# Performance work log

Measured on AMD Instinct MI355X. Metric: run time of the kernel, lower is better.

## Reference

```python
import jax, jax.numpy as jnp
import numpy as np

B = 16384
WIDE_DIM = 256          # 32 wide features * dim 8
DEEP_DIM = 1024         # 64 deep features * embedding_dim 16
SHARED = [2048, 1024, 512]
DOMAIN = [512, 256]
NUM_DOMAINS = 8


def setup_inputs() -> dict:
    key = jax.random.key(0)
    ks = jax.random.split(key, 20)
    s = 0.01  # embedding_init_var-style small init
    inp = {
        "wide_features": jax.random.normal(ks[0], (B, WIDE_DIM), jnp.float32),
        "deep_features": jax.random.normal(ks[1], (B, DEEP_DIM), jnp.float32),
        "domain_ids": jax.random.randint(ks[2], (B,), 0, NUM_DOMAINS, jnp.int64),
        # shared MLP (weights stored [in, out])
        "W1": jax.random.normal(ks[3], (DEEP_DIM, SHARED[0]), jnp.float32) * s,
        "b1": jnp.zeros((SHARED[0],), jnp.float32),
        "W2": jax.random.normal(ks[4], (SHARED[0], SHARED[1]), jnp.float32) * s,
        "b2": jnp.zeros((SHARED[1],), jnp.float32),
        "W3": jax.random.normal(ks[5], (SHARED[1], SHARED[2]), jnp.float32) * s,
        "b3": jnp.zeros((SHARED[2],), jnp.float32),
        # domain-specific MLP
        "Wd1": jax.random.normal(ks[6], (SHARED[2], DOMAIN[0]), jnp.float32) * s,
        "bd1": jnp.zeros((DOMAIN[0],), jnp.float32),
        "Wd2": jax.random.normal(ks[7], (DOMAIN[0], DOMAIN[1]), jnp.float32) * s,
        "bd2": jnp.zeros((DOMAIN[1],), jnp.float32),
        # per-domain output heads: Linear(DOMAIN[-1], 1) per domain
        "Wh": jax.random.normal(ks[8], (NUM_DOMAINS, DOMAIN[1]), jnp.float32) * s,
        "bh": jnp.zeros((NUM_DOMAINS,), jnp.float32),
    }
    return inp


def reference(wide_features, deep_features, domain_ids,
              W1, b1, W2, b2, W3, b3, Wd1, bd1, Wd2, bd2, Wh, bh):
    # wide part: sum embedding output to a scalar logit per sample [B, 1]
    wide = jnp.sum(wide_features, axis=1, keepdims=True)
    # shared deep MLP
    h = jax.nn.relu(deep_features @ W1 + b1)
    h = jax.nn.relu(h @ W2 + b2)
    shared = jax.nn.relu(h @ W3 + b3)          # [B, 512]
    # domain-specific tower (shared across domains)
    d = jax.nn.relu(shared @ Wd1 + bd1)
    d = jax.nn.relu(d @ Wd2 + bd2)             # [B, 256]
    # per-sample domain head routing: gather head weights, fused dot
    w = Wh[domain_ids]                          # [B, 256]
    head = jnp.sum(d * w, axis=1, keepdims=True) + bh[domain_ids][:, None]  # [B, 1]
    out = jax.nn.sigmoid(wide + head)
    return (out, shared, d)
```

## Files before the change

kernel.cpp:

```cpp
#include <hip/hip_runtime.h>
#include <hip/hip_bf16.h>


typedef __attribute__((ext_vector_type(8))) short short8;
typedef __attribute__((ext_vector_type(4))) float f32x4;

static __device__ __forceinline__ unsigned short f2bf_bits(float x) {
  __hip_bfloat16 h = __float2bfloat16(x);
  return __builtin_bit_cast(unsigned short, h);
}
static __device__ __forceinline__ float bf_bits2f(unsigned short u) {
  __hip_bfloat16 h = __builtin_bit_cast(__hip_bfloat16, u);
  return __bfloat162float(h);
}

static __device__ __forceinline__ void gload16(const void* g, void* l) {
  __builtin_amdgcn_global_load_lds(
      (const __attribute__((address_space(1))) void*)g,
      (__attribute__((address_space(3))) void*)l, 16, 0, 0);
}

static __device__ __forceinline__ unsigned lds_u32(const void* p) {
  return (unsigned)(uintptr_t)(const __attribute__((address_space(3))) void*)p;
}

static __device__ __forceinline__ short8 dsr(unsigned addr) {
  short8 r;
  asm volatile("ds_read_b128 %0, %1" : "=v"(r) : "v"(addr));
  return r;
}

#define MFMA16(a, b, c) __builtin_amdgcn_mfma_f32_16x16x32_bf16((a), (b), (c), 0, 0, 0)
#define SB0() __builtin_amdgcn_sched_barrier(0)
#define PRIO(x) __builtin_amdgcn_s_setprio(x)
#define BAR() __builtin_amdgcn_s_barrier()

__global__ void transpose_convert(const float* __restrict__ W,
                                  __hip_bfloat16* __restrict__ Wt,
                                  int K, int N) {
  __shared__ float tile[64][65];
  const int k0 = blockIdx.y * 64;
  const int n0 = blockIdx.x * 64;
  const int t  = threadIdx.x;
  const int tn = t & 63;
  const int t4 = t >> 6;
#pragma unroll
  for (int p = 0; p < 16; ++p) {
    int kl = p * 4 + t4;
    tile[kl][tn] = W[(size_t)(k0 + kl) * N + (n0 + tn)];
  }
  __syncthreads();
#pragma unroll
  for (int p = 0; p < 16; ++p) {
    int nl = p * 4 + t4;
    Wt[(size_t)(n0 + nl) * K + (k0 + tn)] = __float2bfloat16(tile[tn][nl]);
  }
}

__global__ void f32_to_bf16(const float* __restrict__ in,
                            unsigned short* __restrict__ out, int n8) {
  int i = blockIdx.x * blockDim.x + threadIdx.x;
  if (i >= n8) return;
  const f32x4* p = (const f32x4*)in + (size_t)i * 2;
  f32x4 a = p[0], b = p[1];
  short8 o;
  o[0] = (short)f2bf_bits(a[0]); o[1] = (short)f2bf_bits(a[1]);
  o[2] = (short)f2bf_bits(a[2]); o[3] = (short)f2bf_bits(a[3]);
  o[4] = (short)f2bf_bits(b[0]); o[5] = (short)f2bf_bits(b[1]);
  o[6] = (short)f2bf_bits(b[2]); o[7] = (short)f2bf_bits(b[3]);
  *(short8*)(out + (size_t)i * 8) = o;
}

__global__ __launch_bounds__(512, 2) void gemm_8p(
    const __hip_bfloat16* __restrict__ A,
    const __hip_bfloat16* __restrict__ Bt,
    const float* __restrict__ bias,
    __hip_bfloat16* __restrict__ Cb,
    float* __restrict__ Cf,
    int N, int K, int nbx) {
  __shared__ char lds[131072];

  const int tid  = threadIdx.x;
  const int lane = tid & 63;
  const int wid  = tid >> 6;
  const int wm   = wid >> 2;
  const int wn   = wid & 3;

  const int nwg = gridDim.x;
  const int cpx = nwg >> 3;
  const int id  = blockIdx.x;
  const int swz = (id & 7) * cpx + (id >> 3);
  const int bm  = (swz / nbx) * 256;
  const int bn  = (swz % nbx) * 256;

  const int ln15 = lane & 15;
  const unsigned cswz = (unsigned)((((lane >> 4) ^ (lane & 7)) << 4));

  const unsigned lbase = lds_u32(lds);
  const unsigned arow0 = lbase + (unsigned)(wm * 128 + ln15) * 128u + cswz;
  const unsigned brow0 = lbase + 32768u + (unsigned)(wn * 64 + ln15) * 128u + cswz;

  const int nt = K >> 6;

  const int swc = (tid & 7) ^ ((tid >> 3) & 7);
  const __hip_bfloat16* baseA = A  + (size_t)(bm + (tid >> 3)) * K + swc * 8;
  const __hip_bfloat16* baseB = Bt + (size_t)(bn + (tid >> 3)) * K + swc * 8;
  const unsigned ldst0 = (unsigned)(wid * 1024);

  auto stage = [&](int kt, int half, int isB) {
    const __hip_bfloat16* base = isB ? baseB : baseA;
    char* dst = lds + ((kt & 1) * 65536) + (isB ? 32768 : 0) + half * 16384;
#pragma unroll
    for (int q = 0; q < 2; ++q) {
      gload16(base + (size_t)((half * 128 + q * 64) * K + kt * 64),
              dst + q * 8192 + ldst0);
    }
  };

  f32x4 acc[8][4] = {};

  stage(0, 0, 1); stage(0, 0, 0); stage(0, 1, 1); stage(0, 1, 0);
  if (nt > 1) { stage(1, 0, 1); stage(1, 0, 0); }

  for (int t = 0; t < nt; ++t) {
    const unsigned po = (unsigned)(t & 1) * 65536u;
    short8 a_[4][2], b0_[2][2], b1_[2][2];

    if (t + 1 < nt) asm volatile("s_waitcnt vmcnt(4)");
    else            asm volatile("s_waitcnt vmcnt(0)");
    BAR();
#pragma unroll
    for (int mi = 0; mi < 4; ++mi) a_[mi][0] = dsr(arow0 + po + (unsigned)(mi * 2048));
#pragma unroll
    for (int nj = 0; nj < 2; ++nj) b0_[nj][0] = dsr(brow0 + po + (unsigned)(nj * 2048));
#pragma unroll
    for (int mi = 0; mi < 4; ++mi) a_[mi][1] = dsr((arow0 + po + (unsigned)(mi * 2048)) ^ 64u);
#pragma unroll
    for (int nj = 0; nj < 2; ++nj) b0_[nj][1] = dsr((brow0 + po + (unsigned)(nj * 2048)) ^ 64u);
    if (t + 1 < nt) stage(t + 1, 1, 1);
    asm volatile("s_waitcnt lgkmcnt(6)");
    SB0();
    PRIO(1);
#pragma unroll
    for (int mi = 0; mi < 4; ++mi)
#pragma unroll
      for (int nj = 0; nj < 2; ++nj)
        acc[mi][nj] = MFMA16(a_[mi][0], b0_[nj][0], acc[mi][nj]);
    asm volatile("s_waitcnt lgkmcnt(0)");
    SB0();
#pragma unroll
    for (int mi = 0; mi < 4; ++mi)
#pragma unroll
      for (int nj = 0; nj < 2; ++nj)
        acc[mi][nj] = MFMA16(a_[mi][1], b0_[nj][1], acc[mi][nj]);
    PRIO(0);

#pragma unroll
    for (int nj = 0; nj < 2; ++nj) {
      unsigned bd = brow0 + po + (unsigned)((nj + 2) * 2048);
      b1_[nj][0] = dsr(bd); b1_[nj][1] = dsr(bd ^ 64u);
    }
    if (t + 1 < nt) stage(t + 1, 1, 0);
    BAR();
    asm volatile("s_waitcnt lgkmcnt(0)");
    SB0();
    PRIO(1);
#pragma unroll
    for (int kk = 0; kk < 2; ++kk)
#pragma unroll
      for (int mi = 0; mi < 4; ++mi)
#pragma unroll
        for (int nj = 0; nj < 2; ++nj)
          acc[mi][nj + 2] = MFMA16(a_[mi][kk], b1_[nj][kk], acc[mi][nj + 2]);
    PRIO(0);

#pragma unroll
    for (int mi = 0; mi < 4; ++mi) {
      unsigned ad = arow0 + po + (unsigned)((mi + 4) * 2048);
      a_[mi][0] = dsr(ad); a_[mi][1] = dsr(ad ^ 64u);
    }
    BAR();
    if (t + 2 < nt) stage(t + 2, 0, 1);
    asm volatile("s_waitcnt lgkmcnt(0)");
    SB0();
    PRIO(1);
#pragma unroll
    for (int kk = 0; kk < 2; ++kk)
#pragma unroll
      for (int mi = 0; mi < 4; ++mi)
#pragma unroll
        for (int nj = 0; nj < 2; ++nj)
          acc[mi + 4][nj] = MFMA16(a_[mi][kk], b0_[nj][kk], acc[mi + 4][nj]);
    PRIO(0);

    BAR();
    if (t + 2 < nt) stage(t + 2, 0, 0);
    PRIO(1);
#pragma unroll
    for (int kk = 0; kk < 2; ++kk)
#pragma unroll
      for (int mi = 0; mi < 4; ++mi)
#pragma unroll
        for (int nj = 0; nj < 2; ++nj)
          acc[mi + 4][nj + 2] = MFMA16(a_[mi][kk], b1_[nj][kk], acc[mi + 4][nj + 2]);
    PRIO(0);
  }

  float biasv[4];
#pragma unroll
  for (int nj = 0; nj < 4; ++nj)
    biasv[nj] = bias[bn + wn * 64 + nj * 16 + ln15];

#pragma unroll
  for (int mi = 0; mi < 8; ++mi) {
    int row0 = bm + wm * 128 + mi * 16 + (lane >> 4) * 4;
#pragma unroll
    for (int nj = 0; nj < 4; ++nj) {
      int col = bn + wn * 64 + nj * 16 + ln15;
#pragma unroll
      for (int r = 0; r < 4; ++r) {
        float v = acc[mi][nj][r] + biasv[nj];
        v = v > 0.f ? v : 0.f;
        size_t idx = (size_t)(row0 + r) * N + col;
        Cb[idx] = __float2bfloat16(v);
        if (Cf) Cf[idx] = v;
      }
    }
  }
}

__global__ __launch_bounds__(512, 2) void gemm_8pq(
    const __hip_bfloat16* __restrict__ A,
    const __hip_bfloat16* __restrict__ Bt,
    const float* __restrict__ bias,
    __hip_bfloat16* __restrict__ Cb,
    int N, int K, int nbx) {
  __shared__ char lds[131072];

  const int tid  = threadIdx.x;
  const int lane = tid & 63;
  const int wid  = tid >> 6;
  const int wm   = wid >> 2;
  const int wn   = wid & 3;

  const int nwg = gridDim.x;
  const int cpx = nwg >> 3;
  const int id  = blockIdx.x;
  const int swz = (id & 7) * cpx + (id >> 3);
  const int bm  = (swz / nbx) * 256;
  const int bn  = (swz % nbx) * 256;

  const int ln15 = lane & 15;
  const unsigned cswz = (unsigned)((((lane >> 4) ^ (lane & 7)) << 4));

  const unsigned lbase = lds_u32(lds);
  const unsigned arow0 = lbase + (unsigned)(wm * 128 + ln15) * 128u + cswz;
  const unsigned brow0 = lbase + 32768u + (unsigned)(wn * 64 + ln15) * 128u + cswz;

  const int nt = K >> 6;

  const int swc = (tid & 7) ^ ((tid >> 3) & 7);
  const __hip_bfloat16* baseA = A  + (size_t)(bm + (tid >> 3)) * K + swc * 8;
  const __hip_bfloat16* baseB = Bt + (size_t)(bn + (tid >> 3)) * K + swc * 8;
  const unsigned ldst0 = (unsigned)(wid * 1024);

  auto stage = [&](int kt, int half, int isB) {
    const __hip_bfloat16* base = isB ? baseB : baseA;
    char* dst = lds + ((kt & 1) * 65536) + (isB ? 32768 : 0) + half * 16384;
#pragma unroll
    for (int q = 0; q < 2; ++q) {
      gload16(base + (size_t)((half * 128 + q * 64) * K + kt * 64),
              dst + q * 8192 + ldst0);
    }
  };

  f32x4 acc[8][4] = {};
  short8 aLo[4][2], aHi[4][2], b0v[2][2], b1v[2][2];

  stage(0, 0, 1); stage(0, 0, 0); stage(0, 1, 1); stage(0, 1, 0);
  if (nt > 1) {
    stage(1, 0, 1); stage(1, 0, 0);
    asm volatile("s_waitcnt vmcnt(4)");
  } else {
    asm volatile("s_waitcnt vmcnt(0)");
  }
  BAR();
#pragma unroll
  for (int mi = 0; mi < 4; ++mi) {
    unsigned ad = arow0 + (unsigned)(mi * 2048);
    aLo[mi][0] = dsr(ad); aLo[mi][1] = dsr(ad ^ 64u);
  }

  for (int t = 0; t < nt; ++t) {
    const unsigned po = (unsigned)(t & 1) * 65536u;
    const unsigned pn = po ^ 65536u;

    asm volatile("s_waitcnt lgkmcnt(0)");
    SB0();
#pragma unroll
    for (int nj = 0; nj < 2; ++nj) b0v[nj][0] = dsr(brow0 + po + (unsigned)(nj * 2048));
#pragma unroll
    for (int nj = 0; nj < 2; ++nj) b0v[nj][1] = dsr((brow0 + po + (unsigned)(nj * 2048)) ^ 64u);
#pragma unroll
    for (int nj = 0; nj < 2; ++nj) b1v[nj][0] = dsr(brow0 + po + (unsigned)((nj + 2) * 2048));
#pragma unroll
    for (int nj = 0; nj < 2; ++nj) b1v[nj][1] = dsr((brow0 + po + (unsigned)((nj + 2) * 2048)) ^ 64u);
    asm volatile("s_waitcnt lgkmcnt(6)");
    SB0();
    PRIO(1);
#pragma unroll
    for (int mi = 0; mi < 4; ++mi)
#pragma unroll
      for (int nj = 0; nj < 2; ++nj)
        acc[mi][nj] = MFMA16(aLo[mi][0], b0v[nj][0], acc[mi][nj]);
    asm volatile("s_waitcnt lgkmcnt(4)");
    SB0();
#pragma unroll
    for (int mi = 0; mi < 4; ++mi)
#pragma unroll
      for (int nj = 0; nj < 2; ++nj)
        acc[mi][nj] = MFMA16(aLo[mi][1], b0v[nj][1], acc[mi][nj]);
    PRIO(0);
    if (t + 1 < nt) stage(t + 1, 1, 1);
    BAR();

    asm volatile("s_waitcnt lgkmcnt(0)");
    SB0();
#pragma unroll
    for (int mi = 0; mi < 4; ++mi) {
      unsigned ad = arow0 + po + (unsigned)((mi + 4) * 2048);
      aHi[mi][0] = dsr(ad); aHi[mi][1] = dsr(ad ^ 64u);
    }
    PRIO(1);
#pragma unroll
    for (int kk = 0; kk < 2; ++kk)
#pragma unroll
      for (int mi = 0; mi < 4; ++mi)
#pragma unroll
        for (int nj = 0; nj < 2; ++nj)
          acc[mi][nj + 2] = MFMA16(aLo[mi][kk], b1v[nj][kk], acc[mi][nj + 2]);
    PRIO(0);
    if (t + 1 < nt) stage(t + 1, 1, 0);
    BAR();

    asm volatile("s_waitcnt lgkmcnt(0)");
    SB0();
    PRIO(1);
#pragma unroll
    for (int kk = 0; kk < 2; ++kk)
#pragma unroll
      for (int mi = 0; mi < 4; ++mi)
#pragma unroll
        for (int nj = 0; nj < 2; ++nj)
          acc[mi + 4][nj] = MFMA16(aHi[mi][kk], b0v[nj][kk], acc[mi + 4][nj]);
    PRIO(0);
    if (t + 2 < nt) stage(t + 2, 0, 1);
    if (t + 1 < nt) {
      if (t + 2 < nt) asm volatile("s_waitcnt vmcnt(2)");
      else            asm volatile("s_waitcnt vmcnt(0)");
    }
    BAR();

    SB0();
    if (t + 1 < nt) {
#pragma unroll
      for (int mi = 0; mi < 4; ++mi) {
        unsigned ad = arow0 + pn + (unsigned)(mi * 2048);
        aLo[mi][0] = dsr(ad); aLo[mi][1] = dsr(ad ^ 64u);
      }
    }
    PRIO(1);
#pragma unroll
    for (int kk = 0; kk < 2; ++kk)
#pragma unroll
      for (int mi = 0; mi < 4; ++mi)
#pragma unroll
        for (int nj = 0; nj < 2; ++nj)
          acc[mi + 4][nj + 2] = MFMA16(aHi[mi][kk], b1v[nj][kk], acc[mi + 4][nj + 2]);
    PRIO(0);
    if (t + 2 < nt) stage(t + 2, 0, 0);
    BAR();
  }

  float biasv[4];
#pragma unroll
  for (int nj = 0; nj < 4; ++nj)
    biasv[nj] = bias[bn + wn * 64 + nj * 16 + ln15];

#pragma unroll
  for (int mi = 0; mi < 8; ++mi) {
    int row0 = bm + wm * 128 + mi * 16 + (lane >> 4) * 4;
#pragma unroll
    for (int nj = 0; nj < 4; ++nj) {
      int col = bn + wn * 64 + nj * 16 + ln15;
#pragma unroll
      for (int r = 0; r < 4; ++r) {
        float v = acc[mi][nj][r] + biasv[nj];
        v = v > 0.f ? v : 0.f;
        Cb[(size_t)(row0 + r) * N + col] = __float2bfloat16(v);
      }
    }
  }
}

__global__ __launch_bounds__(512, 2) void gemm_128(
    const __hip_bfloat16* __restrict__ A,
    const __hip_bfloat16* __restrict__ Bt,
    const float* __restrict__ bias,
    __hip_bfloat16* __restrict__ Cb,
    float* __restrict__ Cf,
    int N, int K, int nbx) {
  __shared__ char lds[98304];

  const int tid  = threadIdx.x;
  const int lane = tid & 63;
  const int wid  = tid >> 6;
  const int wm   = wid >> 2;
  const int wn   = wid & 3;

  const int nwg = gridDim.x;
  const int cpx = nwg >> 3;
  const int id  = blockIdx.x;
  const int swz = (id & 7) * cpx + (id >> 3);
  const int bm  = (swz / nbx) * 128;
  const int bn  = (swz % nbx) * 256;

  const int ln15 = lane & 15;
  const unsigned cswz = (unsigned)((((lane >> 4) ^ (lane & 7)) << 4));

  const unsigned lbase = lds_u32(lds);
  const unsigned arow0 = lbase + (unsigned)(wm * 64 + ln15) * 128u + cswz;
  const unsigned brow0 = lbase + 16384u + (unsigned)(wn * 64 + ln15) * 128u + cswz;

  const int nt = K >> 6;

  const int swc = (tid & 7) ^ ((tid >> 3) & 7);
  const __hip_bfloat16* baseA = A  + (size_t)(bm + (tid >> 3)) * K + swc * 8;
  const __hip_bfloat16* baseB = Bt + (size_t)(bn + (tid >> 3)) * K + swc * 8;
  const unsigned ldst0 = (unsigned)(tid * 16);

  auto stageA = [&](int kt, int half) {
    char* dst = lds + ((kt & 1) * 49152) + half * 8192;
    gload16(baseA + (size_t)((half * 64) * K + kt * 64), dst + ldst0);
  };
  auto stageB = [&](int kt, int half) {
    char* dst = lds + ((kt & 1) * 49152) + 16384 + half * 16384;
#pragma unroll
    for (int q = 0; q < 2; ++q) {
      gload16(baseB + (size_t)((half * 128 + q * 64) * K + kt * 64),
              dst + q * 8192 + ldst0);
    }
  };

  f32x4 acc[4][4] = {};

  stageB(0, 0); stageA(0, 0); stageB(0, 1); stageA(0, 1);
  if (nt > 1) { stageB(1, 0); stageA(1, 0); }

  for (int t = 0; t < nt; ++t) {
    const unsigned po = (unsigned)(t & 1) * 49152u;
    short8 a_[4][2], b_[4][2];

    if (t + 1 < nt) asm volatile("s_waitcnt vmcnt(3)");
    else            asm volatile("s_waitcnt vmcnt(0)");
    BAR();
#pragma unroll
    for (int mi = 0; mi < 2; ++mi) a_[mi][0] = dsr(arow0 + po + (unsigned)(mi * 2048));
#pragma unroll
    for (int nj = 0; nj < 2; ++nj) b_[nj][0] = dsr(brow0 + po + (unsigned)(nj * 2048));
#pragma unroll
    for (int mi = 0; mi < 2; ++mi) a_[mi][1] = dsr((arow0 + po + (unsigned)(mi * 2048)) ^ 64u);
#pragma unroll
    for (int nj = 0; nj < 2; ++nj) b_[nj][1] = dsr((brow0 + po + (unsigned)(nj * 2048)) ^ 64u);
    if (t + 1 < nt) stageB(t + 1, 1);
    asm volatile("s_waitcnt lgkmcnt(4)");
    SB0();
    PRIO(1);
#pragma unroll
    for (int mi = 0; mi < 2; ++mi)
#pragma unroll
      for (int nj = 0; nj < 2; ++nj)
        acc[mi][nj] = MFMA16(a_[mi][0], b_[nj][0], acc[mi][nj]);
    asm volatile("s_waitcnt lgkmcnt(0)");
    SB0();
#pragma unroll
    for (int mi = 0; mi < 2; ++mi)
#pragma unroll
      for (int nj = 0; nj < 2; ++nj)
        acc[mi][nj] = MFMA16(a_[mi][1], b_[nj][1], acc[mi][nj]);
    PRIO(0);

#pragma unroll
    for (int nj = 0; nj < 2; ++nj) {
      unsigned bd = brow0 + po + (unsigned)((nj + 2) * 2048);
      b_[nj + 2][0] = dsr(bd); b_[nj + 2][1] = dsr(bd ^ 64u);
    }
    if (t + 1 < nt) stageA(t + 1, 1);
    BAR();
    asm volatile("s_waitcnt lgkmcnt(0)");
    SB0();
    PRIO(1);
#pragma unroll
    for (int kk = 0; kk < 2; ++kk)
#pragma unroll
      for (int mi = 0; mi < 2; ++mi)
#pragma unroll
        for (int nj = 0; nj < 2; ++nj)
          acc[mi][nj + 2] = MFMA16(a_[mi][kk], b_[nj + 2][kk], acc[mi][nj + 2]);
    PRIO(0);

#pragma unroll
    for (int mi = 0; mi < 2; ++mi) {
      unsigned ad = arow0 + po + (unsigned)((mi + 2) * 2048);
      a_[mi + 2][0] = dsr(ad); a_[mi + 2][1] = dsr(ad ^ 64u);
    }
    BAR();
    if (t + 2 < nt) stageB(t + 2, 0);
    asm volatile("s_waitcnt lgkmcnt(0)");
    SB0();
    PRIO(1);
#pragma unroll
    for (int kk = 0; kk < 2; ++kk)
#pragma unroll
      for (int mi = 0; mi < 2; ++mi)
#pragma unroll
        for (int nj = 0; nj < 2; ++nj)
          acc[mi + 2][nj] = MFMA16(a_[mi + 2][kk], b_[nj][kk], acc[mi + 2][nj]);
    PRIO(0);

    BAR();
    if (t + 2 < nt) stageA(t + 2, 0);
    PRIO(1);
#pragma unroll
    for (int kk = 0; kk < 2; ++kk)
#pragma unroll
      for (int mi = 0; mi < 2; ++mi)
#pragma unroll
        for (int nj = 0; nj < 2; ++nj)
          acc[mi + 2][nj + 2] = MFMA16(a_[mi + 2][kk], b_[nj + 2][kk], acc[mi + 2][nj + 2]);
    PRIO(0);
  }

  float biasv[4];
#pragma unroll
  for (int nj = 0; nj < 4; ++nj)
    biasv[nj] = bias[bn + wn * 64 + nj * 16 + ln15];

#pragma unroll
  for (int mi = 0; mi < 4; ++mi) {
    int row0 = bm + wm * 64 + mi * 16 + (lane >> 4) * 4;
#pragma unroll
    for (int nj = 0; nj < 4; ++nj) {
      int col = bn + wn * 64 + nj * 16 + ln15;
#pragma unroll
      for (int r = 0; r < 4; ++r) {
        float v = acc[mi][nj][r] + biasv[nj];
        v = v > 0.f ? v : 0.f;
        size_t idx = (size_t)(row0 + r) * N + col;
        Cb[idx] = __float2bfloat16(v);
        if (Cf) Cf[idx] = v;
      }
    }
  }
}

__global__ __launch_bounds__(256, 2) void gemm_bt(
    const __hip_bfloat16* __restrict__ A,
    const __hip_bfloat16* __restrict__ Bt,
    const float* __restrict__ bias,
    __hip_bfloat16* __restrict__ Cb,
    float* __restrict__ Cf,
    int N, int K) {
  __shared__ char lds[32768];

  const int tid  = threadIdx.x;
  const int lane = tid & 63;
  const int wid  = tid >> 6;
  const int wm   = wid >> 1;
  const int wn   = wid & 1;
  const int bm   = blockIdx.y * 128;
  const int bn   = blockIdx.x * 128;

  f32x4 acc[4][4] = {};

  const int srow = tid >> 3;
  const int sk   = (tid & 7) * 8;
  const int kTiles = K >> 6;

  for (int kt = 0; kt < kTiles; ++kt) {
    __syncthreads();
    const __hip_bfloat16* ga = A  + (size_t)(bm + srow) * K + kt * 64 + sk;
    const __hip_bfloat16* gb = Bt + (size_t)(bn + srow) * K + kt * 64 + sk;
#pragma unroll
    for (int p = 0; p < 4; ++p) {
      gload16(ga + (size_t)(p * 32) * K, &lds[p * 4096 + wid * 1024]);
      gload16(gb + (size_t)(p * 32) * K, &lds[16384 + p * 4096 + wid * 1024]);
    }
    __syncthreads();

#pragma unroll
    for (int kk = 0; kk < 2; ++kk) {
      short8 avec[4], bvec[4];
#pragma unroll
      for (int i = 0; i < 4; ++i) {
        int row = wm * 64 + i * 16 + (lane & 15);
        avec[i] = *(const short8*)&lds[row * 128 + kk * 64 + (lane >> 4) * 16];
      }
#pragma unroll
      for (int j = 0; j < 4; ++j) {
        int row = wn * 64 + j * 16 + (lane & 15);
        bvec[j] = *(const short8*)&lds[16384 + row * 128 + kk * 64 + (lane >> 4) * 16];
      }
#pragma unroll
      for (int i = 0; i < 4; ++i)
#pragma unroll
        for (int j = 0; j < 4; ++j)
          acc[i][j] = MFMA16(avec[i], bvec[j], acc[i][j]);
    }
  }

  float biasv[4];
#pragma unroll
  for (int j = 0; j < 4; ++j)
    biasv[j] = bias[bn + wn * 64 + j * 16 + (lane & 15)];

#pragma unroll
  for (int i = 0; i < 4; ++i) {
    int row0 = bm + wm * 64 + i * 16 + (lane >> 4) * 4;
#pragma unroll
    for (int j = 0; j < 4; ++j) {
      int col = bn + wn * 64 + j * 16 + (lane & 15);
#pragma unroll
      for (int r = 0; r < 4; ++r) {
        float v = acc[i][j][r] + biasv[j];
        v = v > 0.f ? v : 0.f;
        size_t idx = (size_t)(row0 + r) * N + col;
        Cb[idx] = __float2bfloat16(v);
        if (Cf) Cf[idx] = v;
      }
    }
  }
}

__global__ __launch_bounds__(256) void head_kernel(
    const float* __restrict__ wide,
    const __hip_bfloat16* __restrict__ D,
    const int* __restrict__ dom,
    const float* __restrict__ Wh,
    const float* __restrict__ bh,
    float* __restrict__ out, int B) {
  const int wid  = threadIdx.x >> 6;
  const int lane = threadIdx.x & 63;
  const int row  = blockIdx.x * 4 + wid;
  if (row >= B) return;
  const int dm = dom[row];

  f32x4 wv = ((const f32x4*)(wide + (size_t)row * 256))[lane];
  float tot = wv[0] + wv[1] + wv[2] + wv[3];

  const unsigned short* drow = (const unsigned short*)(D + (size_t)row * 256);
  ushort4 dv = ((const ushort4*)drow)[lane];
  f32x4 hv = ((const f32x4*)(Wh + (size_t)dm * 256))[lane];
  tot += bf_bits2f(dv.x) * hv[0] + bf_bits2f(dv.y) * hv[1] +
         bf_bits2f(dv.z) * hv[2] + bf_bits2f(dv.w) * hv[3];

#pragma unroll
  for (int off = 32; off > 0; off >>= 1) tot += __shfl_xor(tot, off);

  if (lane == 0) {
    float x = tot + bh[dm];
    out[row] = 1.f / (1.f + __expf(-x));
  }
}

extern "C" void kernel_launch(void* const* d_in, const int* in_sizes, int n_in,
                              void* d_out, int out_size, void* d_ws, size_t ws_size,
                              hipStream_t stream) {
  const float* wide = (const float*)d_in[0];
  const float* deep = (const float*)d_in[1];
  const int*   dom  = (const int*)d_in[2];
  const float* W1  = (const float*)d_in[3];
  const float* b1  = (const float*)d_in[4];
  const float* W2  = (const float*)d_in[5];
  const float* b2  = (const float*)d_in[6];
  const float* W3  = (const float*)d_in[7];
  const float* b3  = (const float*)d_in[8];
  const float* Wd1 = (const float*)d_in[9];
  const float* bd1 = (const float*)d_in[10];
  const float* Wd2 = (const float*)d_in[11];
  const float* bd2 = (const float*)d_in[12];
  const float* Wh  = (const float*)d_in[13];
  const float* bh  = (const float*)d_in[14];
  float* out = (float*)d_out;

  const int B = 16384;
  char* ws = (char*)d_ws;
  __hip_bfloat16* buf0 = (__hip_bfloat16*)ws;
  __hip_bfloat16* buf1 = (__hip_bfloat16*)(ws + 33554432ull);
  __hip_bfloat16* W1t  = (__hip_bfloat16*)(ws + 100663296ull);
  __hip_bfloat16* W2t  = W1t + 2048 * 1024;
  __hip_bfloat16* W3t  = W2t + 1024 * 2048;
  __hip_bfloat16* Wd1t = W3t + 512 * 1024;
  __hip_bfloat16* Wd2t = Wd1t + 512 * 512;

  transpose_convert<<<dim3(2048 / 64, 1024 / 64), 256, 0, stream>>>(W1, W1t, 1024, 2048);
  transpose_convert<<<dim3(1024 / 64, 2048 / 64), 256, 0, stream>>>(W2, W2t, 2048, 1024);
  transpose_convert<<<dim3(512 / 64, 1024 / 64), 256, 0, stream>>>(W3, W3t, 1024, 512);
  transpose_convert<<<dim3(512 / 64, 512 / 64), 256, 0, stream>>>(Wd1, Wd1t, 512, 512);
  transpose_convert<<<dim3(256 / 64, 512 / 64), 256, 0, stream>>>(Wd2, Wd2t, 512, 256);

  {
    int n8 = B * 1024 / 8;
    f32_to_bf16<<<(n8 + 255) / 256, 256, 0, stream>>>(deep, (unsigned short*)buf0, n8);
  }

  float* shared_out = out + B;
  float* d_out_f    = out + B + (size_t)B * 512;

  gemm_8p<<<dim3((2048 / 256) * (B / 256)), 512, 0, stream>>>(
      buf0, W1t, b1, buf1, nullptr, 2048, 1024, 2048 / 256);
  gemm_8pq<<<dim3((1024 / 256) * (B / 256)), 512, 0, stream>>>(
      buf1, W2t, b2, buf0, 1024, 2048, 1024 / 256);
  gemm_128<<<dim3((B / 128) * (512 / 256)), 512, 0, stream>>>(
      buf0, W3t, b3, buf1, shared_out, 512, 1024, 512 / 256);
  gemm_128<<<dim3((B / 128) * (512 / 256)), 512, 0, stream>>>(
      buf1, Wd1t, bd1, buf0, nullptr, 512, 512, 512 / 256);
  gemm_bt<<<dim3(256 / 128, B / 128), 256, 0, stream>>>(buf0, Wd2t, bd2, buf1, d_out_f, 256, 512);

  head_kernel<<<B / 4, 256, 0, stream>>>(wide, buf1, dom, Wh, bh, out, B);
}
```

Baseline: 227.3 us.

## Restructure GEMM main loops to two barriers per k-step with cross-iteration A prefetch

```diff
diff --git a/kernel.cpp b/kernel.cpp
--- a/kernel.cpp
+++ b/kernel.cpp
@@ -71,7 +71,7 @@
   *(short8*)(out + (size_t)i * 8) = o;
 }
 
-__global__ __launch_bounds__(512, 2) void gemm_8p(
+__global__ __launch_bounds__(512, 2) void gemm_2b(
     const __hip_bfloat16* __restrict__ A,
     const __hip_bfloat16* __restrict__ Bt,
     const float* __restrict__ bias,
@@ -118,25 +118,36 @@
   };
 
   f32x4 acc[8][4] = {};
+  short8 aLo[4][2], aHi[4][2], b0v[2][2], b1v[2][2];
 
   stage(0, 0, 1); stage(0, 0, 0); stage(0, 1, 1); stage(0, 1, 0);
-  if (nt > 1) { stage(1, 0, 1); stage(1, 0, 0); }
+  if (nt > 1) {
+    stage(1, 0, 1); stage(1, 0, 0);
+    asm volatile("s_waitcnt vmcnt(4)");
+  } else {
+    asm volatile("s_waitcnt vmcnt(0)");
+  }
+  BAR();
+#pragma unroll
+  for (int mi = 0; mi < 4; ++mi) {
+    unsigned ad = arow0 + (unsigned)(mi * 2048);
+    aLo[mi][0] = dsr(ad); aLo[mi][1] = dsr(ad ^ 64u);
+  }
 
   for (int t = 0; t < nt; ++t) {
     const unsigned po = (unsigned)(t & 1) * 65536u;
-    short8 a_[4][2], b0_[2][2], b1_[2][2];
-
-    if (t + 1 < nt) asm volatile("s_waitcnt vmcnt(4)");
-    else            asm volatile("s_waitcnt vmcnt(0)");
-    BAR();
-#pragma unroll
-    for (int mi = 0; mi < 4; ++mi) a_[mi][0] = dsr(arow0 + po + (unsigned)(mi * 2048));
-#pragma unroll
-    for (int nj = 0; nj < 2; ++nj) b0_[nj][0] = dsr(brow0 + po + (unsigned)(nj * 2048));
-#pragma unroll
-    for (int mi = 0; mi < 4; ++mi) a_[mi][1] = dsr((arow0 + po + (unsigned)(mi * 2048)) ^ 64u);
-#pragma unroll
-    for (int nj = 0; nj < 2; ++nj) b0_[nj][1] = dsr((brow0 + po + (unsigned)(nj * 2048)) ^ 64u);
+    const unsigned pn = po ^ 65536u;
+
+    asm volatile("s_waitcnt lgkmcnt(0)");
+    SB0();
+#pragma unroll
+    for (int nj = 0; nj < 2; ++nj) b0v[nj][0] = dsr(brow0 + po + (unsigned)(nj * 2048));
+#pragma unroll
+    for (int nj = 0; nj < 2; ++nj) b0v[nj][1] = dsr((brow0 + po + (unsigned)(nj * 2048)) ^ 64u);
+#pragma unroll
+    for (int nj = 0; nj < 2; ++nj) b1v[nj][0] = dsr(brow0 + po + (unsigned)((nj + 2) * 2048));
+#pragma unroll
+    for (int nj = 0; nj < 2; ++nj) b1v[nj][1] = dsr((brow0 + po + (unsigned)((nj + 2) * 2048)) ^ 64u);
     if (t + 1 < nt) stage(t + 1, 1, 1);
     asm volatile("s_waitcnt lgkmcnt(6)");
     SB0();
@@ -145,43 +156,58 @@
     for (int mi = 0; mi < 4; ++mi)
 #pragma unroll
       for (int nj = 0; nj < 2; ++nj)
-        acc[mi][nj] = MFMA16(a_[mi][0], b0_[nj][0], acc[mi][nj]);
-    asm volatile("s_waitcnt lgkmcnt(0)");
+        acc[mi][nj] = MFMA16(aLo[mi][0], b0v[nj][0], acc[mi][nj]);
+    asm volatile("s_waitcnt lgkmcnt(4)");
     SB0();
 #pragma unroll
     for (int mi = 0; mi < 4; ++mi)
 #pragma unroll
       for (int nj = 0; nj < 2; ++nj)
-        acc[mi][nj] = MFMA16(a_[mi][1], b0_[nj][1], acc[mi][nj]);
-    PRIO(0);
-
-#pragma unroll
-    for (int nj = 0; nj < 2; ++nj) {
-      unsigned bd = brow0 + po + (unsigned)((nj + 2) * 2048);
-      b1_[nj][0] = dsr(bd); b1_[nj][1] = dsr(bd ^ 64u);
-    }
-    if (t + 1 < nt) stage(t + 1, 1, 0);
-    BAR();
-    asm volatile("s_waitcnt lgkmcnt(0)");
-    SB0();
-    PRIO(1);
-#pragma unroll
-    for (int kk = 0; kk < 2; ++kk)
-#pragma unroll
-      for (int mi = 0; mi < 4; ++mi)
-#pragma unroll
-        for (int nj = 0; nj < 2; ++nj)
-          acc[mi][nj + 2] = MFMA16(a_[mi][kk], b1_[nj][kk], acc[mi][nj + 2]);
+        acc[mi][nj] = MFMA16(aLo[mi][1], b0v[nj][1], acc[mi][nj]);
     PRIO(0);
 
 #pragma unroll
     for (int mi = 0; mi < 4; ++mi) {
       unsigned ad = arow0 + po + (unsigned)((mi + 4) * 2048);
-      a_[mi][0] = dsr(ad); a_[mi][1] = dsr(ad ^ 64u);
-    }
+      aHi[mi][0] = dsr(ad); aHi[mi][1] = dsr(ad ^ 64u);
+    }
+    if (t + 1 < nt) stage(t + 1, 1, 0);
+    asm volatile("s_waitcnt lgkmcnt(8)");
+    SB0();
+    PRIO(1);
+#pragma unroll
+    for (int kk = 0; kk < 2; ++kk)
+#pragma unroll
+      for (int mi = 0; mi < 4; ++mi)
+#pragma unroll
+        for (int nj = 0; nj < 2; ++nj)
+          acc[mi][nj + 2] = MFMA16(aLo[mi][kk], b1v[nj][kk], acc[mi][nj + 2]);
+    PRIO(0);
     BAR();
+
+    asm volatile("s_waitcnt lgkmcnt(0)");
+    SB0();
+    PRIO(1);
+#pragma unroll
+    for (int kk = 0; kk < 2; ++kk)
+#pragma unroll
+      for (int mi = 0; mi < 4; ++mi)
+#pragma unroll
+        for (int nj = 0; nj < 2; ++nj)
+          acc[mi + 4][nj] = MFMA16(aHi[mi][kk], b0v[nj][kk], acc[mi + 4][nj]);
+    PRIO(0);
     if (t + 2 < nt) stage(t + 2, 0, 1);
-    asm volatile("s_waitcnt lgkmcnt(0)");
+    if (t + 2 < nt)      asm volatile("s_waitcnt vmcnt(2)");
+    else if (t + 1 < nt) asm volatile("s_waitcnt vmcnt(0)");
+    if (t + 1 < nt) BAR();
+
+    if (t + 1 < nt) {
+#pragma unroll
+      for (int mi = 0; mi < 4; ++mi) {
+        unsigned ad = arow0 + pn + (unsigned)(mi * 2048);
+        aLo[mi][0] = dsr(ad); aLo[mi][1] = dsr(ad ^ 64u);
+      }
+    }
     SB0();
     PRIO(1);
 #pragma unroll
@@ -190,20 +216,9 @@
       for (int mi = 0; mi < 4; ++mi)
 #pragma unroll
         for (int nj = 0; nj < 2; ++nj)
-          acc[mi + 4][nj] = MFMA16(a_[mi][kk], b0_[nj][kk], acc[mi + 4][nj]);
-    PRIO(0);
-
-    BAR();
+          acc[mi + 4][nj + 2] = MFMA16(aHi[mi][kk], b1v[nj][kk], acc[mi + 4][nj + 2]);
+    PRIO(0);
     if (t + 2 < nt) stage(t + 2, 0, 0);
-    PRIO(1);
-#pragma unroll
-    for (int kk = 0; kk < 2; ++kk)
-#pragma unroll
-      for (int mi = 0; mi < 4; ++mi)
-#pragma unroll
-        for (int nj = 0; nj < 2; ++nj)
-          acc[mi + 4][nj + 2] = MFMA16(a_[mi][kk], b1_[nj][kk], acc[mi + 4][nj + 2]);
-    PRIO(0);
   }
 
   float biasv[4];
@@ -224,180 +239,6 @@
         size_t idx = (size_t)(row0 + r) * N + col;
         Cb[idx] = __float2bfloat16(v);
         if (Cf) Cf[idx] = v;
-      }
-    }
-  }
-}
-
-__global__ __launch_bounds__(512, 2) void gemm_8pq(
-    const __hip_bfloat16* __restrict__ A,
-    const __hip_bfloat16* __restrict__ Bt,
-    const float* __restrict__ bias,
-    __hip_bfloat16* __restrict__ Cb,
-    int N, int K, int nbx) {
-  __shared__ char lds[131072];
-
-  const int tid  = threadIdx.x;
-  const int lane = tid & 63;
-  const int wid  = tid >> 6;
-  const int wm   = wid >> 2;
-  const int wn   = wid & 3;
-
-  const int nwg = gridDim.x;
-  const int cpx = nwg >> 3;
-  const int id  = blockIdx.x;
-  const int swz = (id & 7) * cpx + (id >> 3);
-  const int bm  = (swz / nbx) * 256;
-  const int bn  = (swz % nbx) * 256;
-
-  const int ln15 = lane & 15;
-  const unsigned cswz = (unsigned)((((lane >> 4) ^ (lane & 7)) << 4));
-
-  const unsigned lbase = lds_u32(lds);
-  const unsigned arow0 = lbase + (unsigned)(wm * 128 + ln15) * 128u + cswz;
-  const unsigned brow0 = lbase + 32768u + (unsigned)(wn * 64 + ln15) * 128u + cswz;
-
-  const int nt = K >> 6;
-
-  const int swc = (tid & 7) ^ ((tid >> 3) & 7);
-  const __hip_bfloat16* baseA = A  + (size_t)(bm + (tid >> 3)) * K + swc * 8;
-  const __hip_bfloat16* baseB = Bt + (size_t)(bn + (tid >> 3)) * K + swc * 8;
-  const unsigned ldst0 = (unsigned)(wid * 1024);
-
-  auto stage = [&](int kt, int half, int isB) {
-    const __hip_bfloat16* base = isB ? baseB : baseA;
-    char* dst = lds + ((kt & 1) * 65536) + (isB ? 32768 : 0) + half * 16384;
-#pragma unroll
-    for (int q = 0; q < 2; ++q) {
-      gload16(base + (size_t)((half * 128 + q * 64) * K + kt * 64),
-              dst + q * 8192 + ldst0);
-    }
-  };
-
-  f32x4 acc[8][4] = {};
-  short8 aLo[4][2], aHi[4][2], b0v[2][2], b1v[2][2];
-
-  stage(0, 0, 1); stage(0, 0, 0); stage(0, 1, 1); stage(0, 1, 0);
-  if (nt > 1) {
-    stage(1, 0, 1); stage(1, 0, 0);
-    asm volatile("s_waitcnt vmcnt(4)");
-  } else {
-    asm volatile("s_waitcnt vmcnt(0)");
-  }
-  BAR();
-#pragma unroll
-  for (int mi = 0; mi < 4; ++mi) {
-    unsigned ad = arow0 + (unsigned)(mi * 2048);
-    aLo[mi][0] = dsr(ad); aLo[mi][1] = dsr(ad ^ 64u);
-  }
-
-  for (int t = 0; t < nt; ++t) {
-    const unsigned po = (unsigned)(t & 1) * 65536u;
-    const unsigned pn = po ^ 65536u;
-
-    asm volatile("s_waitcnt lgkmcnt(0)");
-    SB0();
-#pragma unroll
-    for (int nj = 0; nj < 2; ++nj) b0v[nj][0] = dsr(brow0 + po + (unsigned)(nj * 2048));
-#pragma unroll
-    for (int nj = 0; nj < 2; ++nj) b0v[nj][1] = dsr((brow0 + po + (unsigned)(nj * 2048)) ^ 64u);
-#pragma unroll
-    for (int nj = 0; nj < 2; ++nj) b1v[nj][0] = dsr(brow0 + po + (unsigned)((nj + 2) * 2048));
-#pragma unroll
-    for (int nj = 0; nj < 2; ++nj) b1v[nj][1] = dsr((brow0 + po + (unsigned)((nj + 2) * 2048)) ^ 64u);
-    asm volatile("s_waitcnt lgkmcnt(6)");
-    SB0();
-    PRIO(1);
-#pragma unroll
-    for (int mi = 0; mi < 4; ++mi)
-#pragma unroll
-      for (int nj = 0; nj < 2; ++nj)
-        acc[mi][nj] = MFMA16(aLo[mi][0], b0v[nj][0], acc[mi][nj]);
-    asm volatile("s_waitcnt lgkmcnt(4)");
-    SB0();
-#pragma unroll
-    for (int mi = 0; mi < 4; ++mi)
-#pragma unroll
-      for (int nj = 0; nj < 2; ++nj)
-        acc[mi][nj] = MFMA16(aLo[mi][1], b0v[nj][1], acc[mi][nj]);
-    PRIO(0);
-    if (t + 1 < nt) stage(t + 1, 1, 1);
-    BAR();
-
-    asm volatile("s_waitcnt lgkmcnt(0)");
-    SB0();
-#pragma unroll
-    for (int mi = 0; mi < 4; ++mi) {
-      unsigned ad = arow0 + po + (unsigned)((mi + 4) * 2048);
-      aHi[mi][0] = dsr(ad); aHi[mi][1] = dsr(ad ^ 64u);
-    }
-    PRIO(1);
-#pragma unroll
-    for (int kk = 0; kk < 2; ++kk)
-#pragma unroll
-      for (int mi = 0; mi < 4; ++mi)
-#pragma unroll
-        for (int nj = 0; nj < 2; ++nj)
-          acc[mi][nj + 2] = MFMA16(aLo[mi][kk], b1v[nj][kk], acc[mi][nj + 2]);
-    PRIO(0);
-    if (t + 1 < nt) stage(t + 1, 1, 0);
-    BAR();
-
-    asm volatile("s_waitcnt lgkmcnt(0)");
-    SB0();
-    PRIO(1);
-#pragma unroll
-    for (int kk = 0; kk < 2; ++kk)
-#pragma unroll
-      for (int mi = 0; mi < 4; ++mi)
-#pragma unroll
-        for (int nj = 0; nj < 2; ++nj)
-          acc[mi + 4][nj] = MFMA16(aHi[mi][kk], b0v[nj][kk], acc[mi + 4][nj]);
-    PRIO(0);
-    if (t + 2 < nt) stage(t + 2, 0, 1);
-    if (t + 1 < nt) {
-      if (t + 2 < nt) asm volatile("s_waitcnt vmcnt(2)");
-      else            asm volatile("s_waitcnt vmcnt(0)");
-    }
-    BAR();
-
-    SB0();
-    if (t + 1 < nt) {
-#pragma unroll
-      for (int mi = 0; mi < 4; ++mi) {
-        unsigned ad = arow0 + pn + (unsigned)(mi * 2048);
-        aLo[mi][0] = dsr(ad); aLo[mi][1] = dsr(ad ^ 64u);
-      }
-    }
-    PRIO(1);
-#pragma unroll
-    for (int kk = 0; kk < 2; ++kk)
-#pragma unroll
-      for (int mi = 0; mi < 4; ++mi)
-#pragma unroll
-        for (int nj = 0; nj < 2; ++nj)
-          acc[mi + 4][nj + 2] = MFMA16(aHi[mi][kk], b1v[nj][kk], acc[mi + 4][nj + 2]);
-    PRIO(0);
-    if (t + 2 < nt) stage(t + 2, 0, 0);
-    BAR();
-  }
-
-  float biasv[4];
-#pragma unroll
-  for (int nj = 0; nj < 4; ++nj)
-    biasv[nj] = bias[bn + wn * 64 + nj * 16 + ln15];
-
-#pragma unroll
-  for (int mi = 0; mi < 8; ++mi) {
-    int row0 = bm + wm * 128 + mi * 16 + (lane >> 4) * 4;
-#pragma unroll
-    for (int nj = 0; nj < 4; ++nj) {
-      int col = bn + wn * 64 + nj * 16 + ln15;
-#pragma unroll
-      for (int r = 0; r < 4; ++r) {
-        float v = acc[mi][nj][r] + biasv[nj];
-        v = v > 0.f ? v : 0.f;
-        Cb[(size_t)(row0 + r) * N + col] = __float2bfloat16(v);
       }
     }
   }
@@ -453,70 +294,96 @@
   };
 
   f32x4 acc[4][4] = {};
+  short8 aLo[2][2], aHi[2][2], b0v[2][2], b1v[2][2];
 
   stageB(0, 0); stageA(0, 0); stageB(0, 1); stageA(0, 1);
-  if (nt > 1) { stageB(1, 0); stageA(1, 0); }
+  if (nt > 1) {
+    stageB(1, 0); stageA(1, 0);
+    asm volatile("s_waitcnt vmcnt(3)");
+  } else {
+    asm volatile("s_waitcnt vmcnt(0)");
+  }
+  BAR();
+#pragma unroll
+  for (int mi = 0; mi < 2; ++mi) {
+    unsigned ad = arow0 + (unsigned)(mi * 2048);
+    aLo[mi][0] = dsr(ad); aLo[mi][1] = dsr(ad ^ 64u);
+  }
 
   for (int t = 0; t < nt; ++t) {
     const unsigned po = (unsigned)(t & 1) * 49152u;
-    short8 a_[4][2], b_[4][2];
-
-    if (t + 1 < nt) asm volatile("s_waitcnt vmcnt(3)");
-    else            asm volatile("s_waitcnt vmcnt(0)");
-    BAR();
-#pragma unroll
-    for (int mi = 0; mi < 2; ++mi) a_[mi][0] = dsr(arow0 + po + (unsigned)(mi * 2048));
-#pragma unroll
-    for (int nj = 0; nj < 2; ++nj) b_[nj][0] = dsr(brow0 + po + (unsigned)(nj * 2048));
-#pragma unroll
-    for (int mi = 0; mi < 2; ++mi) a_[mi][1] = dsr((arow0 + po + (unsigned)(mi * 2048)) ^ 64u);
-#pragma unroll
-    for (int nj = 0; nj < 2; ++nj) b_[nj][1] = dsr((brow0 + po + (unsigned)(nj * 2048)) ^ 64u);
+    const unsigned pn = po ^ 49152u;
+
+    asm volatile("s_waitcnt lgkmcnt(0)");
+    SB0();
+#pragma unroll
+    for (int nj = 0; nj < 2; ++nj) b0v[nj][0] = dsr(brow0 + po + (unsigned)(nj * 2048));
+#pragma unroll
+    for (int nj = 0; nj < 2; ++nj) b0v[nj][1] = dsr((brow0 + po + (unsigned)(nj * 2048)) ^ 64u);
+#pragma unroll
+    for (int nj = 0; nj < 2; ++nj) b1v[nj][0] = dsr(brow0 + po + (unsigned)((nj + 2) * 2048));
+#pragma unroll
+    for (int nj = 0; nj < 2; ++nj) b1v[nj][1] = dsr((brow0 + po + (unsigned)((nj + 2) * 2048)) ^ 64u);
     if (t + 1 < nt) stageB(t + 1, 1);
+    asm volatile("s_waitcnt lgkmcnt(6)");
+    SB0();
+    PRIO(1);
+#pragma unroll
+    for (int mi = 0; mi < 2; ++mi)
+#pragma unroll
+      for (int nj = 0; nj < 2; ++nj)
+        acc[mi][nj] = MFMA16(aLo[mi][0], b0v[nj][0], acc[mi][nj]);
     asm volatile("s_waitcnt lgkmcnt(4)");
     SB0();
-    PRIO(1);
 #pragma unroll
     for (int mi = 0; mi < 2; ++mi)
 #pragma unroll
       for (int nj = 0; nj < 2; ++nj)
-        acc[mi][nj] = MFMA16(a_[mi][0], b_[nj][0], acc[mi][nj]);
-    asm volatile("s_waitcnt lgkmcnt(0)");
-    SB0();
-#pragma unroll
-    for (int mi = 0; mi < 2; ++mi)
-#pragma unroll
-      for (int nj = 0; nj < 2; ++nj)
-        acc[mi][nj] = MFMA16(a_[mi][1], b_[nj][1], acc[mi][nj]);
-    PRIO(0);
-
-#pragma unroll
-    for (int nj = 0; nj < 2; ++nj) {
-      unsigned bd = brow0 + po + (unsigned)((nj + 2) * 2048);
-      b_[nj + 2][0] = dsr(bd); b_[nj + 2][1] = dsr(bd ^ 64u);
-    }
-    if (t + 1 < nt) stageA(t + 1, 1);
-    BAR();
-    asm volatile("s_waitcnt lgkmcnt(0)");
-    SB0();
-    PRIO(1);
-#pragma unroll
-    for (int kk = 0; kk < 2; ++kk)
-#pragma unroll
-      for (int mi = 0; mi < 2; ++mi)
-#pragma unroll
-        for (int nj = 0; nj < 2; ++nj)
-          acc[mi][nj + 2] = MFMA16(a_[mi][kk], b_[nj + 2][kk], acc[mi][nj + 2]);
+        acc[mi][nj] = MFMA16(aLo[mi][1], b0v[nj][1], acc[mi][nj]);
     PRIO(0);
 
 #pragma unroll
     for (int mi = 0; mi < 2; ++mi) {
       unsigned ad = arow0 + po + (unsigned)((mi + 2) * 2048);
-      a_[mi + 2][0] = dsr(ad); a_[mi + 2][1] = dsr(ad ^ 64u);
-    }
+      aHi[mi][0] = dsr(ad); aHi[mi][1] = dsr(ad ^ 64u);
+    }
+    if (t + 1 < nt) stageA(t + 1, 1);
+    asm volatile("s_waitcnt lgkmcnt(4)");
+    SB0();
+    PRIO(1);
+#pragma unroll
+    for (int kk = 0; kk < 2; ++kk)
+#pragma unroll
+      for (int mi = 0; mi < 2; ++mi)
+#pragma unroll
+        for (int nj = 0; nj < 2; ++nj)
+          acc[mi][nj + 2] = MFMA16(aLo[mi][kk], b1v[nj][kk], acc[mi][nj + 2]);
+    PRIO(0);
     BAR();
+
+    asm volatile("s_waitcnt lgkmcnt(0)");
+    SB0();
+    PRIO(1);
+#pragma unroll
+    for (int kk = 0; kk < 2; ++kk)
+#pragma unroll
+      for (int mi = 0; mi < 2; ++mi)
+#pragma unroll
+        for (int nj = 0; nj < 2; ++nj)
+          acc[mi + 2][nj] = MFMA16(aHi[mi][kk], b0v[nj][kk], acc[mi + 2][nj]);
+    PRIO(0);
     if (t + 2 < nt) stageB(t + 2, 0);
-    asm volatile("s_waitcnt lgkmcnt(0)");
+    if (t + 2 < nt)      asm volatile("s_waitcnt vmcnt(2)");
+    else if (t + 1 < nt) asm volatile("s_waitcnt vmcnt(0)");
+    if (t + 1 < nt) BAR();
+
+    if (t + 1 < nt) {
+#pragma unroll
+      for (int mi = 0; mi < 2; ++mi) {
+        unsigned ad = arow0 + pn + (unsigned)(mi * 2048);
+        aLo[mi][0] = dsr(ad); aLo[mi][1] = dsr(ad ^ 64u);
+      }
+    }
     SB0();
     PRIO(1);
 #pragma unroll
@@ -525,20 +392,9 @@
       for (int mi = 0; mi < 2; ++mi)
 #pragma unroll
         for (int nj = 0; nj < 2; ++nj)
-          acc[mi + 2][nj] = MFMA16(a_[mi + 2][kk], b_[nj][kk], acc[mi + 2][nj]);
-    PRIO(0);
-
-    BAR();
+          acc[mi + 2][nj + 2] = MFMA16(aHi[mi][kk], b1v[nj][kk], acc[mi + 2][nj + 2]);
+    PRIO(0);
     if (t + 2 < nt) stageA(t + 2, 0);
-    PRIO(1);
-#pragma unroll
-    for (int kk = 0; kk < 2; ++kk)
-#pragma unroll
-      for (int mi = 0; mi < 2; ++mi)
-#pragma unroll
-        for (int nj = 0; nj < 2; ++nj)
-          acc[mi + 2][nj + 2] = MFMA16(a_[mi + 2][kk], b_[nj + 2][kk], acc[mi + 2][nj + 2]);
-    PRIO(0);
   }
 
   float biasv[4];
@@ -717,10 +573,10 @@
   float* shared_out = out + B;
   float* d_out_f    = out + B + (size_t)B * 512;
 
-  gemm_8p<<<dim3((2048 / 256) * (B / 256)), 512, 0, stream>>>(
+  gemm_2b<<<dim3((2048 / 256) * (B / 256)), 512, 0, stream>>>(
       buf0, W1t, b1, buf1, nullptr, 2048, 1024, 2048 / 256);
-  gemm_8pq<<<dim3((1024 / 256) * (B / 256)), 512, 0, stream>>>(
-      buf1, W2t, b2, buf0, 1024, 2048, 1024 / 256);
+  gemm_2b<<<dim3((1024 / 256) * (B / 256)), 512, 0, stream>>>(
+      buf1, W2t, b2, buf0, nullptr, 1024, 2048, 1024 / 256);
   gemm_128<<<dim3((B / 128) * (512 / 256)), 512, 0, stream>>>(
       buf0, W3t, b3, buf1, shared_out, 512, 1024, 512 / 256);
   gemm_128<<<dim3((B / 128) * (512 / 256)), 512, 0, stream>>>(
```

New measurement: 224.4 us. About the same (-1.3%).
